# Kernel optimization log

Measured on AMD Instinct MI355X. Metric: run time of the kernel, lower is better.

The kernel has to match this reference:

```python
import jax, jax.numpy as jnp
import numpy as np

N, E, F_IN, H, G, C = 200000, 1000000, 64, 64, 512, 10
EPS = 1e-5


def setup_inputs() -> dict:
    key = jax.random.key(0)
    ks = jax.random.split(key, 16)
    x = jax.random.normal(ks[0], (N, F_IN), dtype=jnp.float32)
    edge_index = jax.random.randint(ks[1], (2, E), 0, N, dtype=jnp.int32)
    batch = jnp.sort(jax.random.randint(ks[2], (N,), 0, G, dtype=jnp.int32))
    def glorot(k, shape):
        lim = np.sqrt(6.0 / (shape[0] + shape[1]))
        return jax.random.uniform(k, shape, jnp.float32, -lim, lim)
    return {
        "x": x, "edge_index": edge_index, "batch": batch,
        "W1": glorot(ks[3], (F_IN, H)), "b1": jnp.zeros((H,), jnp.float32),
        "g1": jnp.ones((H,), jnp.float32), "be1": jnp.zeros((H,), jnp.float32),
        "W2": glorot(ks[4], (H, H)), "b2": jnp.zeros((H,), jnp.float32),
        "g2": jnp.ones((H,), jnp.float32), "be2": jnp.zeros((H,), jnp.float32),
        "lw1": glorot(ks[5], (H, H // 2)), "lb1": jnp.zeros((H // 2,), jnp.float32),
        "lw2": glorot(ks[6], (H // 2, C)), "lb2": jnp.zeros((C,), jnp.float32),
    }


def _gcn_conv(h, src, dst, norm, W, b):
    # PyG GCNConv: linear transform, then normalized gather-scatter aggregation
    h = h @ W                                   # [N, H]
    msg = h[src] * norm[:, None]                # [E+N, H] gather + scale
    out = jax.ops.segment_sum(msg, dst, num_segments=N)  # scatter-add
    return out + b


def _bn_relu(h, g, be):
    m = h.mean(axis=0)
    v = jnp.var(h, axis=0)                      # biased var, as torch BN training
    return jax.nn.relu((h - m) * jax.lax.rsqrt(v + EPS) * g + be)


def reference(x, edge_index, batch, W1, b1, g1, be1, W2, b2, g2, be2,
              lw1, lb1, lw2, lb2):
    loop = jnp.arange(N, dtype=edge_index.dtype)
    src = jnp.concatenate([edge_index[0], loop])  # add self-loops
    dst = jnp.concatenate([edge_index[1], loop])
    deg = jax.ops.segment_sum(jnp.ones_like(src, jnp.float32), dst, num_segments=N)
    dinv = jax.lax.rsqrt(jnp.maximum(deg, 1.0))
    norm = dinv[src] * dinv[dst]                  # sym normalization

    h = _bn_relu(_gcn_conv(x, src, dst, norm, W1, b1), g1, be1)
    prev = h
    h = _bn_relu(_gcn_conv(h, src, dst, norm, W2, b2), g2, be2)
    h = h + prev                                  # residual (dims match)

    # global mean pool over graphs
    sums = jax.ops.segment_sum(h, batch, num_segments=G)        # [G, H]
    cnt = jax.ops.segment_sum(jnp.ones((N,), jnp.float32), batch, num_segments=G)
    pooled = sums / jnp.maximum(cnt, 1.0)[:, None]

    z = jax.nn.relu(pooled @ lw1 + lb1)
    logits = z @ lw2 + lb2                        # [G, C]
    return jax.nn.log_softmax(logits, axis=-1)
```

## Files before the change

kernel.cpp:

```cpp
#include <hip/hip_runtime.h>
#include <hip/hip_bf16.h>
#include <cstdint>
#include <cstddef>

typedef unsigned short u16;
typedef unsigned int u32;
typedef __attribute__((ext_vector_type(8))) short bf16x8;
typedef __attribute__((ext_vector_type(4))) float f32x4;

__device__ __forceinline__ float bf2f(u16 u) {
    return __uint_as_float(((u32)u) << 16);
}
__device__ __forceinline__ float bflo(u32 u) { return __uint_as_float(u << 16); }
__device__ __forceinline__ float bfhi(u32 u) { return __uint_as_float(u & 0xFFFF0000u); }
__device__ __forceinline__ u32 f2bf(float f) {
    u32 b = __float_as_uint(f);
    return (b + 0x7FFFu + ((b >> 16) & 1u)) >> 16;
}

#define CAP 32


__global__ void k_bfill(const int* __restrict__ ei, int E, int N,
                        int* __restrict__ cnt, int* __restrict__ bucket) {
    int e = blockIdx.x * blockDim.x + threadIdx.x;
    if (e >= E) return;
    int s = ei[e], d = ei[E + e];
    int pos = atomicAdd(&cnt[d], 1);
    if (pos < CAP) bucket[(size_t)pos * N + d] = s;
}


__global__ __launch_bounds__(256) void k_gemm1(
        const float* __restrict__ X, const float* __restrict__ W,
        const int* __restrict__ cnt, u16* __restrict__ Yb, int nrows) {
    int lane = threadIdx.x & 63;
    int wave = threadIdx.x >> 6;
    int row0 = blockIdx.x * 64 + wave * 16;
    if (row0 >= nrows) return;
    int lrow = lane & 15;
    int lgrp = lane >> 4;

    bf16x8 bfrag[4][2];
#pragma unroll
    for (int c = 0; c < 4; ++c)
#pragma unroll
        for (int h = 0; h < 2; ++h) {
            bf16x8 t;
#pragma unroll
            for (int j = 0; j < 8; ++j)
                t[j] = (short)f2bf(W[(h * 32 + lgrp * 8 + j) * 64 + c * 16 + lrow]);
            bfrag[c][h] = t;
        }

    int arow = min(row0 + lrow, nrows - 1);
    const float* xr = X + (size_t)arow * 64 + lgrp * 8;
    bf16x8 afrag[2];
#pragma unroll
    for (int h = 0; h < 2; ++h) {
        bf16x8 t;
#pragma unroll
        for (int j = 0; j < 8; ++j) t[j] = (short)f2bf(xr[h * 32 + j]);
        afrag[h] = t;
    }

    f32x4 acc[4] = {};
#pragma unroll
    for (int h = 0; h < 2; ++h)
#pragma unroll
        for (int c = 0; c < 4; ++c)
            acc[c] = __builtin_amdgcn_mfma_f32_16x16x32_bf16(afrag[h], bfrag[c][h], acc[c], 0, 0, 0);

#pragma unroll
    for (int j = 0; j < 4; ++j) {
        int r = row0 + lgrp * 4 + j;
        if (r < nrows) {
            float dv = rsqrtf((float)(cnt[r] + 1));
#pragma unroll
            for (int c = 0; c < 4; ++c)
                Yb[(size_t)r * 64 + c * 16 + lrow] = (u16)f2bf(acc[c][j] * dv);
        }
    }
}


__global__ __launch_bounds__(256) void k_gemm2(
        const u16* __restrict__ Xb, const float* __restrict__ W,
        const float* __restrict__ st, const float* __restrict__ g,
        const float* __restrict__ be, const int* __restrict__ cnt,
        u16* __restrict__ Yb, int nrows) {
    __shared__ float ssc[128];
    if (threadIdx.x < 64) {
        int f = threadIdx.x;
        float invn = 1.f / (float)nrows;
        float m   = st[f] * invn;
        float var = st[64 + f] * invn - m * m;
        float scale = g[f] * rsqrtf(var + 1e-5f);
        ssc[f]      = scale;
        ssc[64 + f] = be[f] - m * scale;
    }
    __syncthreads();

    int lane = threadIdx.x & 63;
    int wave = threadIdx.x >> 6;
    int row0 = blockIdx.x * 64 + wave * 16;
    if (row0 >= nrows) return;
    int lrow = lane & 15;
    int lgrp = lane >> 4;

    bf16x8 bfrag[4][2];
#pragma unroll
    for (int c = 0; c < 4; ++c)
#pragma unroll
        for (int h = 0; h < 2; ++h) {
            bf16x8 t;
#pragma unroll
            for (int j = 0; j < 8; ++j)
                t[j] = (short)f2bf(W[(h * 32 + lgrp * 8 + j) * 64 + c * 16 + lrow]);
            bfrag[c][h] = t;
        }

    int arow = min(row0 + lrow, nrows - 1);
    const u16* xr = Xb + (size_t)arow * 64 + lgrp * 8;
    bf16x8 afrag[2];
#pragma unroll
    for (int h = 0; h < 2; ++h) {
        bf16x8 t;
#pragma unroll
        for (int j = 0; j < 8; ++j) {
            int k = h * 32 + lgrp * 8 + j;
            float v = bf2f(xr[h * 32 + j]);
            v = fmaxf(fmaf(v, ssc[k], ssc[64 + k]), 0.f);
            t[j] = (short)f2bf(v);
        }
        afrag[h] = t;
    }

    f32x4 acc[4] = {};
#pragma unroll
    for (int h = 0; h < 2; ++h)
#pragma unroll
        for (int c = 0; c < 4; ++c)
            acc[c] = __builtin_amdgcn_mfma_f32_16x16x32_bf16(afrag[h], bfrag[c][h], acc[c], 0, 0, 0);

#pragma unroll
    for (int j = 0; j < 4; ++j) {
        int r = row0 + lgrp * 4 + j;
        if (r < nrows) {
            float dv = rsqrtf((float)(cnt[r] + 1));
#pragma unroll
            for (int c = 0; c < 4; ++c)
                Yb[(size_t)r * 64 + c * 16 + lrow] = (u16)f2bf(acc[c][j] * dv);
        }
    }
}


__global__ __launch_bounds__(256) void k_gather(
        const u16* __restrict__ HA, const int* __restrict__ cnt,
        const int* __restrict__ bucket, u16* __restrict__ outb,
        float* __restrict__ st, int N) {
    int lane = threadIdx.x & 63;
    int wid  = (blockIdx.x * blockDim.x + threadIdx.x) >> 6;
    int nw   = (gridDim.x * blockDim.x) >> 6;
    float s_ = 0.f, sq_ = 0.f;
    int nb4 = (N + 3) >> 2;
    u32 nm1 = (u32)(N - 1);
    for (int bt = wid; bt < nb4; bt += nw) {
        int r0 = __builtin_amdgcn_readfirstlane(bt << 2);
        int r1 = min(r0 + 1, N - 1);
        int r2 = min(r0 + 2, N - 1);
        int r3 = min(r0 + 3, N - 1);
        int c0 = cnt[r0], c1 = cnt[r1], c2 = cnt[r2], c3 = cnt[r3];
        int n0 = min(c0, CAP), n1 = min(c1, CAP), n2 = min(c2, CAP), n3 = min(c3, CAP);
        float a0 = bf2f(HA[(size_t)r0 * 64 + lane]);
        float a1 = bf2f(HA[(size_t)r1 * 64 + lane]);
        float a2 = bf2f(HA[(size_t)r2 * 64 + lane]);
        float a3 = bf2f(HA[(size_t)r3 * 64 + lane]);
        int nmax = max(max(n0, n1), max(n2, n3));
        for (int c = 0; c < nmax; c += 8) {
#define SLOT(K) int4 q##K = *(const int4*)(bucket + (size_t)(c + K) * N + r0);
            SLOT(0) SLOT(1) SLOT(2) SLOT(3) SLOT(4) SLOT(5) SLOT(6) SLOT(7)
#undef SLOT
#define EDGE(K, I) \
            u32 id##K##I = (c + K < n##I) ? (u32)((&q##K.x)[I]) : 0u; \
            id##K##I = min(id##K##I, nm1); \
            float v##K##I = bf2f(HA[(size_t)id##K##I * 64 + lane]);
            EDGE(0,0) EDGE(0,1) EDGE(0,2) EDGE(0,3)
            EDGE(1,0) EDGE(1,1) EDGE(1,2) EDGE(1,3)
            EDGE(2,0) EDGE(2,1) EDGE(2,2) EDGE(2,3)
            EDGE(3,0) EDGE(3,1) EDGE(3,2) EDGE(3,3)
            EDGE(4,0) EDGE(4,1) EDGE(4,2) EDGE(4,3)
            EDGE(5,0) EDGE(5,1) EDGE(5,2) EDGE(5,3)
            EDGE(6,0) EDGE(6,1) EDGE(6,2) EDGE(6,3)
            EDGE(7,0) EDGE(7,1) EDGE(7,2) EDGE(7,3)
#undef EDGE
#define ACCUM(K, I) a##I += (c + K < n##I) ? v##K##I : 0.f;
            ACCUM(0,0) ACCUM(1,0) ACCUM(2,0) ACCUM(3,0)
            ACCUM(4,0) ACCUM(5,0) ACCUM(6,0) ACCUM(7,0)
            ACCUM(0,1) ACCUM(1,1) ACCUM(2,1) ACCUM(3,1)
            ACCUM(4,1) ACCUM(5,1) ACCUM(6,1) ACCUM(7,1)
            ACCUM(0,2) ACCUM(1,2) ACCUM(2,2) ACCUM(3,2)
            ACCUM(4,2) ACCUM(5,2) ACCUM(6,2) ACCUM(7,2)
            ACCUM(0,3) ACCUM(1,3) ACCUM(2,3) ACCUM(3,3)
            ACCUM(4,3) ACCUM(5,3) ACCUM(6,3) ACCUM(7,3)
#undef ACCUM
        }
        float d0 = rsqrtf((float)(c0 + 1));
        float d1 = rsqrtf((float)(c1 + 1));
        float d2 = rsqrtf((float)(c2 + 1));
        float d3 = rsqrtf((float)(c3 + 1));
        {
            u16 u = (u16)f2bf(a0 * d0);
            outb[(size_t)r0 * 64 + lane] = u;
            float vr = bf2f(u); s_ += vr; sq_ += vr * vr;
        }
        if (r0 + 1 < N) {
            u16 u = (u16)f2bf(a1 * d1);
            outb[(size_t)r1 * 64 + lane] = u;
            float vr = bf2f(u); s_ += vr; sq_ += vr * vr;
        }
        if (r0 + 2 < N) {
            u16 u = (u16)f2bf(a2 * d2);
            outb[(size_t)r2 * 64 + lane] = u;
            float vr = bf2f(u); s_ += vr; sq_ += vr * vr;
        }
        if (r0 + 3 < N) {
            u16 u = (u16)f2bf(a3 * d3);
            outb[(size_t)r3 * 64 + lane] = u;
            float vr = bf2f(u); s_ += vr; sq_ += vr * vr;
        }
    }
    __shared__ float ls[4][64], lq[4][64];
    int grp = threadIdx.x >> 6;
    ls[grp][lane] = s_; lq[grp][lane] = sq_;
    __syncthreads();
    if (grp == 0) {
        s_  = ls[0][lane] + ls[1][lane] + ls[2][lane] + ls[3][lane];
        sq_ = lq[0][lane] + lq[1][lane] + lq[2][lane] + lq[3][lane];
        unsafeAtomicAdd(&st[lane], s_);
        unsafeAtomicAdd(&st[64 + lane], sq_);
    }
}


__global__ void k_pool(const u16* __restrict__ rb2, const float* __restrict__ st2,
                       const float* __restrict__ g2, const float* __restrict__ be2,
                       const u16* __restrict__ rb1, const float* __restrict__ st1,
                       const float* __restrict__ g1, const float* __restrict__ be1,
                       const int* __restrict__ batch, float* __restrict__ psum, int N) {
    __shared__ float s1[128], s2[128];
    if (threadIdx.x < 64) {
        int f = threadIdx.x;
        float invn = 1.f / (float)N;
        float m   = st2[f] * invn;
        float var = st2[64 + f] * invn - m * m;
        float scale = g2[f] * rsqrtf(var + 1e-5f);
        s2[f] = scale; s2[64 + f] = be2[f] - m * scale;
    } else if (threadIdx.x < 128) {
        int f = threadIdx.x - 64;
        float invn = 1.f / (float)N;
        float m   = st1[f] * invn;
        float var = st1[64 + f] * invn - m * m;
        float scale = g1[f] * rsqrtf(var + 1e-5f);
        s1[f] = scale; s1[64 + f] = be1[f] - m * scale;
    }
    __syncthreads();

    int lane = threadIdx.x & 63;
    int wv   = (blockIdx.x * blockDim.x + threadIdx.x) >> 6;
    int r0   = wv * 64;
    if (r0 >= N) return;
    int rend = min(r0 + 64, N);
    int bv = (r0 + lane < N) ? batch[r0 + lane] : -1;
    float s2a = s2[lane], s2b = s2[64 + lane];
    float s1a = s1[lane], s1b = s1[64 + lane];
    float acc = 0.f;
    int cur = __shfl(bv, 0, 64);
    for (int r = r0; r < rend; ++r) {
        int b = __shfl(bv, r - r0, 64);
        if (b != cur) {
            unsafeAtomicAdd(&psum[(size_t)cur * 64 + lane], acc);
            acc = 0.f; cur = b;
        }
        float v2 = fmaxf(fmaf(bf2f(rb2[(size_t)r * 64 + lane]), s2a, s2b), 0.f);
        float v1 = fmaxf(fmaf(bf2f(rb1[(size_t)r * 64 + lane]), s1a, s1b), 0.f);
        acc += v1 + v2;
    }
    unsafeAtomicAdd(&psum[(size_t)cur * 64 + lane], acc);
}


__global__ void k_head(const float* __restrict__ psum, const int* __restrict__ batch,
                       const float* __restrict__ lw1, const float* __restrict__ lb1,
                       const float* __restrict__ lw2, const float* __restrict__ lb2,
                       float* __restrict__ out, int N, int G) {
    int g = blockIdx.x * blockDim.x + threadIdx.x;
    if (g >= G) return;
    int lo = 0, hi = N;
    while (lo < hi) { int mid = (lo + hi) >> 1; if (batch[mid] < g) lo = mid + 1; else hi = mid; }
    int lb = lo;
    hi = N;
    while (lo < hi) { int mid = (lo + hi) >> 1; if (batch[mid] < g + 1) lo = mid + 1; else hi = mid; }
    float cnt = (float)(lo - lb);
    float inv = 1.f / fmaxf(cnt, 1.f);
    float p[64];
#pragma unroll
    for (int f = 0; f < 64; ++f) p[f] = psum[(size_t)g * 64 + f] * inv;
    float z[32];
#pragma unroll
    for (int j = 0; j < 32; ++j) {
        float a = lb1[j];
#pragma unroll
        for (int f = 0; f < 64; ++f) a = fmaf(p[f], lw1[f * 32 + j], a);
        z[j] = fmaxf(a, 0.f);
    }
    float lg[10];
    float mx = -1e30f;
#pragma unroll
    for (int c = 0; c < 10; ++c) {
        float a = lb2[c];
#pragma unroll
        for (int j = 0; j < 32; ++j) a = fmaf(z[j], lw2[j * 10 + c], a);
        lg[c] = a;
        mx = fmaxf(mx, a);
    }
    float se = 0.f;
#pragma unroll
    for (int c = 0; c < 10; ++c) se += expf(lg[c] - mx);
    float lse = logf(se) + mx;
#pragma unroll
    for (int c = 0; c < 10; ++c) out[(size_t)g * 10 + c] = lg[c] - lse;
}


extern "C" void kernel_launch(void* const* d_in, const int* in_sizes, int n_in,
                              void* d_out, int out_size, void* d_ws, size_t ws_size,
                              hipStream_t stream) {
    const float* x    = (const float*)d_in[0];
    const int*   ei   = (const int*)d_in[1];
    const int*   batch= (const int*)d_in[2];
    const float* W1   = (const float*)d_in[3];
    const float* g1   = (const float*)d_in[5];
    const float* be1  = (const float*)d_in[6];
    const float* W2   = (const float*)d_in[7];
    const float* g2   = (const float*)d_in[9];
    const float* be2  = (const float*)d_in[10];
    const float* lw1  = (const float*)d_in[11];
    const float* lb1  = (const float*)d_in[12];
    const float* lw2  = (const float*)d_in[13];
    const float* lb2  = (const float*)d_in[14];
    float* out = (float*)d_out;

    const int N = in_sizes[2];
    const int E = in_sizes[1] / 2;
    const int C = 10;
    const int G = out_size / C;

    char* wp = (char*)d_ws;
    auto carve = [&wp](size_t bytes) -> char* {
        uintptr_t u = ((uintptr_t)wp + 63) & ~(uintptr_t)63;
        char* r = (char*)u;
        wp = r + bytes;
        return r;
    };
    int*   cnt   = (int*)carve((size_t)N * 4);
    float* st1   = (float*)carve(128 * 4);
    float* st2   = (float*)carve(128 * 4);
    float* psum  = (float*)carve((size_t)G * 64 * 4);
    size_t zone  = (char*)(psum + (size_t)G * 64) - (char*)cnt;
    int*   bucket= (int*)carve(((size_t)N * CAP + 16) * 4);
    u16*   HAbf  = (u16*)carve((size_t)N * 64 * 2);
    u16*   Rb1   = (u16*)carve((size_t)N * 64 * 2);
    u16*   Rb2   = (u16*)carve((size_t)N * 64 * 2);

    hipMemsetAsync(cnt, 0, zone, stream);

    const int gemmBlocks = (N + 63) / 64;

    k_bfill<<<(E + 255) / 256, 256, 0, stream>>>(ei, E, N, cnt, bucket);

    k_gemm1<<<gemmBlocks, 256, 0, stream>>>(x, W1, cnt, HAbf, N);
    k_gather<<<4096, 256, 0, stream>>>(HAbf, cnt, bucket, Rb1, st1, N);

    k_gemm2<<<gemmBlocks, 256, 0, stream>>>(Rb1, W2, st1, g1, be1, cnt, HAbf, N);
    k_gather<<<4096, 256, 0, stream>>>(HAbf, cnt, bucket, Rb2, st2, N);

    {
        int waves = (N + 63) / 64;
        int blocks = (waves + 3) / 4;
        k_pool<<<blocks, 256, 0, stream>>>(Rb2, st2, g2, be2, Rb1, st1, g1, be1,
                                           batch, psum, N);
    }

    k_head<<<(G + 255) / 256, 256, 0, stream>>>(psum, batch, lw1, lb1, lw2, lb2,
                                                out, N, G);
}
```

Baseline: 401.1 us.

## Fuse bucket fill with first GEMM and move source-degree scaling into gather

Merges the edge bucketing kernel and the first GEMM into one launch by splitting blocks by index, so the fill and GEMM run concurrently. The GEMM can no longer scale rows by dinv because counts are not final yet, so the first gather reads cnt for every neighbor and applies the source-side rsqrt itself. This saves one launch and lets the GEMM overlap the atomic-heavy fill, at the cost of an extra random cnt load per edge in the first gather. The gather grid also grows from 4096 to 8192 blocks.

After: 604.0 us. 50.6% more time.

```diff
diff --git a/kernel.cpp b/kernel.cpp
--- a/kernel.cpp
+++ b/kernel.cpp
@@ -21,23 +21,25 @@
 #define CAP 32
 
 
-__global__ void k_bfill(const int* __restrict__ ei, int E, int N,
-                        int* __restrict__ cnt, int* __restrict__ bucket) {
-    int e = blockIdx.x * blockDim.x + threadIdx.x;
-    if (e >= E) return;
-    int s = ei[e], d = ei[E + e];
-    int pos = atomicAdd(&cnt[d], 1);
-    if (pos < CAP) bucket[(size_t)pos * N + d] = s;
-}
-
-
-__global__ __launch_bounds__(256) void k_gemm1(
+__global__ __launch_bounds__(256) void k_fused1(
         const float* __restrict__ X, const float* __restrict__ W,
-        const int* __restrict__ cnt, u16* __restrict__ Yb, int nrows) {
+        const int* __restrict__ ei, int E, int N,
+        int* __restrict__ cnt, int* __restrict__ bucket,
+        u16* __restrict__ Yb, int fillBlocks) {
+    if ((int)blockIdx.x < fillBlocks) {
+        int e = blockIdx.x * 256 + threadIdx.x;
+        if (e < E) {
+            int s = ei[e], d = ei[E + e];
+            int pos = atomicAdd(&cnt[d], 1);
+            if (pos < CAP) bucket[(size_t)pos * N + d] = s;
+        }
+        return;
+    }
+    int gb = blockIdx.x - fillBlocks;
     int lane = threadIdx.x & 63;
     int wave = threadIdx.x >> 6;
-    int row0 = blockIdx.x * 64 + wave * 16;
-    if (row0 >= nrows) return;
+    int row0 = gb * 64 + wave * 16;
+    if (row0 >= N) return;
     int lrow = lane & 15;
     int lgrp = lane >> 4;
 
@@ -53,7 +55,7 @@
             bfrag[c][h] = t;
         }
 
-    int arow = min(row0 + lrow, nrows - 1);
+    int arow = min(row0 + lrow, N - 1);
     const float* xr = X + (size_t)arow * 64 + lgrp * 8;
     bf16x8 afrag[2];
 #pragma unroll
@@ -74,12 +76,10 @@
 #pragma unroll
     for (int j = 0; j < 4; ++j) {
         int r = row0 + lgrp * 4 + j;
-        if (r < nrows) {
-            float dv = rsqrtf((float)(cnt[r] + 1));
+        if (r < N)
 #pragma unroll
             for (int c = 0; c < 4; ++c)
-                Yb[(size_t)r * 64 + c * 16 + lrow] = (u16)f2bf(acc[c][j] * dv);
-        }
+                Yb[(size_t)r * 64 + c * 16 + lrow] = (u16)f2bf(acc[c][j]);
     }
 }
 
@@ -156,6 +156,7 @@
 }
 
 
+template <bool NORM>
 __global__ __launch_bounds__(256) void k_gather(
         const u16* __restrict__ HA, const int* __restrict__ cnt,
         const int* __restrict__ bucket, u16* __restrict__ outb,
@@ -173,10 +174,15 @@
         int r3 = min(r0 + 3, N - 1);
         int c0 = cnt[r0], c1 = cnt[r1], c2 = cnt[r2], c3 = cnt[r3];
         int n0 = min(c0, CAP), n1 = min(c1, CAP), n2 = min(c2, CAP), n3 = min(c3, CAP);
+        float d0 = rsqrtf((float)(c0 + 1));
+        float d1 = rsqrtf((float)(c1 + 1));
+        float d2 = rsqrtf((float)(c2 + 1));
+        float d3 = rsqrtf((float)(c3 + 1));
         float a0 = bf2f(HA[(size_t)r0 * 64 + lane]);
         float a1 = bf2f(HA[(size_t)r1 * 64 + lane]);
         float a2 = bf2f(HA[(size_t)r2 * 64 + lane]);
         float a3 = bf2f(HA[(size_t)r3 * 64 + lane]);
+        if (NORM) { a0 *= d0; a1 *= d1; a2 *= d2; a3 *= d3; }
         int nmax = max(max(n0, n1), max(n2, n3));
         for (int c = 0; c < nmax; c += 8) {
 #define SLOT(K) int4 q##K = *(const int4*)(bucket + (size_t)(c + K) * N + r0);
@@ -185,7 +191,8 @@
 #define EDGE(K, I) \
             u32 id##K##I = (c + K < n##I) ? (u32)((&q##K.x)[I]) : 0u; \
             id##K##I = min(id##K##I, nm1); \
-            float v##K##I = bf2f(HA[(size_t)id##K##I * 64 + lane]);
+            float v##K##I = bf2f(HA[(size_t)id##K##I * 64 + lane]); \
+            if (NORM) v##K##I *= rsqrtf((float)(cnt[id##K##I] + 1));
             EDGE(0,0) EDGE(0,1) EDGE(0,2) EDGE(0,3)
             EDGE(1,0) EDGE(1,1) EDGE(1,2) EDGE(1,3)
             EDGE(2,0) EDGE(2,1) EDGE(2,2) EDGE(2,3)
@@ -206,10 +213,6 @@
             ACCUM(4,3) ACCUM(5,3) ACCUM(6,3) ACCUM(7,3)
 #undef ACCUM
         }
-        float d0 = rsqrtf((float)(c0 + 1));
-        float d1 = rsqrtf((float)(c1 + 1));
-        float d2 = rsqrtf((float)(c2 + 1));
-        float d3 = rsqrtf((float)(c3 + 1));
         {
             u16 u = (u16)f2bf(a0 * d0);
             outb[(size_t)r0 * 64 + lane] = u;
@@ -377,14 +380,16 @@
     hipMemsetAsync(cnt, 0, zone, stream);
 
     const int gemmBlocks = (N + 63) / 64;
-
-    k_bfill<<<(E + 255) / 256, 256, 0, stream>>>(ei, E, N, cnt, bucket);
-
-    k_gemm1<<<gemmBlocks, 256, 0, stream>>>(x, W1, cnt, HAbf, N);
-    k_gather<<<4096, 256, 0, stream>>>(HAbf, cnt, bucket, Rb1, st1, N);
+    const int fillBlocks = (E + 255) / 256;
+
+    k_fused1<<<fillBlocks + gemmBlocks, 256, 0, stream>>>(
+        x, W1, ei, E, N, cnt, bucket, HAbf, fillBlocks);
+
+    k_gather<true><<<8192, 256, 0, stream>>>(HAbf, cnt, bucket, Rb1, st1, N);
 
     k_gemm2<<<gemmBlocks, 256, 0, stream>>>(Rb1, W2, st1, g1, be1, cnt, HAbf, N);
-    k_gather<<<4096, 256, 0, stream>>>(HAbf, cnt, bucket, Rb2, st2, N);
+
+    k_gather<false><<<8192, 256, 0, stream>>>(HAbf, cnt, bucket, Rb2, st2, N);
 
     {
         int waves = (N + 63) / 64;
```
